# Optimization experiments

Hardware: AMD Instinct MI355X
Metric: run time of the kernel (lower is better)

## Reference

```python
import jax, jax.numpy as jnp
import numpy as np

N = 100000   # nodes
E = 1000000  # edges (avg degree 10)
F_IN, H1, H2, C = 128, 64, 64, 16


def setup_inputs() -> dict:
    key = jax.random.key(0)
    ks = jax.random.split(key, 10)
    x = jax.random.normal(ks[0], (N, F_IN), dtype=jnp.float32)
    edge_src = jax.random.randint(ks[1], (E,), 0, N, dtype=jnp.int32)
    edge_dst = jax.random.randint(ks[2], (E,), 0, N, dtype=jnp.int32)
    # normalized-adjacency-like positive edge weights (~1/deg scale)
    edge_val = jax.random.uniform(ks[3], (E,), dtype=jnp.float32) * 0.1
    def glorot(k, fan_in, fan_out):
        s = np.float32(1.0 / np.sqrt(fan_in))
        return jax.random.normal(k, (fan_in, fan_out), dtype=jnp.float32) * s
    W1 = glorot(ks[4], F_IN, H1)
    W2 = glorot(ks[5], H1, H2)
    W3 = glorot(ks[6], H2, C)
    b1 = jnp.zeros((H1,), jnp.float32)
    b2 = jnp.zeros((H2,), jnp.float32)
    b3 = jnp.zeros((C,), jnp.float32)
    return {"x": x, "edge_val": edge_val, "W1": W1, "b1": b1,
            "W2": W2, "b2": b2, "W3": W3, "b3": b3,
            "edge_src": edge_src, "edge_dst": edge_dst}


def gcn_layer(h, W, b, edge_src, edge_dst, edge_val):
    # support = h @ W ; out = spmm(adj, support) + b
    support = h @ W                                  # [N, d_out]
    msg = support[edge_src] * edge_val[:, None]      # [E, d_out] gather + scale
    agg = jax.ops.segment_sum(msg, edge_dst, num_segments=N)  # scatter-add
    return agg + b


def reference(x, edge_val, W1, b1, W2, b2, W3, b3, edge_src, edge_dst):
    # eval mode: F.dropout(training=False) is identity
    h = jax.nn.relu(gcn_layer(x, W1, b1, edge_src, edge_dst, edge_val))
    h = jax.nn.relu(gcn_layer(h, W2, b2, edge_src, edge_dst, edge_val))
    return gcn_layer(h, W3, b3, edge_src, edge_dst, edge_val)  # [N, C] logits
```

## Files before the change

kernel.cpp:

```cpp
#include <hip/hip_runtime.h>
#include <stdint.h>

#define N_NODES 100000
#define N_EDGES 1000000
#define NBUCK 98
#define CAP 12288

typedef __attribute__((ext_vector_type(8))) __bf16 bf16x8;
typedef __attribute__((ext_vector_type(4))) float f32x4;

static __device__ __forceinline__ float bf2f(unsigned short u) {
    return __uint_as_float(((unsigned int)u) << 16);
}
static __device__ __forceinline__ unsigned short f2bf(float f) {
    unsigned int u = __float_as_uint(f);
    unsigned int r = (u + 0x7FFFu + ((u >> 16) & 1u)) >> 16;
    return (unsigned short)r;
}
static __device__ __forceinline__ float4 ld4_half(const unsigned short* p) {
    ushort4 u = *(const ushort4*)p;
    return make_float4(bf2f(u.x), bf2f(u.y), bf2f(u.z), bf2f(u.w));
}
static __device__ __forceinline__ void st4_half(unsigned short* p, float4 f) {
    ushort4 u;
    u.x = f2bf(f.x); u.y = f2bf(f.y); u.z = f2bf(f.z); u.w = f2bf(f.w);
    *(ushort4*)p = u;
}
static __device__ __forceinline__ void st8_half(unsigned short* p, const float* f) {
    int4 u;
    u.x = (int)(((unsigned)f2bf(f[0])) | (((unsigned)f2bf(f[1])) << 16));
    u.y = (int)(((unsigned)f2bf(f[2])) | (((unsigned)f2bf(f[3])) << 16));
    u.z = (int)(((unsigned)f2bf(f[4])) | (((unsigned)f2bf(f[5])) << 16));
    u.w = (int)(((unsigned)f2bf(f[6])) | (((unsigned)f2bf(f[7])) << 16));
    *(int4*)p = u;
}

static __device__ __forceinline__ float ldf(const void* p, size_t i, int bf) {
    return bf ? bf2f(((const unsigned short*)p)[i]) : ((const float*)p)[i];
}
static __device__ __forceinline__ float4 ldf4(const void* p, size_t i, int bf) {
    if (bf) return ld4_half((const unsigned short*)p + i);
    return *(const float4*)((const float*)p + i);
}

__global__ __launch_bounds__(256) void detect_kernel(const unsigned short* __restrict__ xs,
                                                     int* __restrict__ flag,
                                                     int* __restrict__ bcursor) {
    __shared__ int sz;
    if (threadIdx.x == 0) sz = 0;
    __syncthreads();
    int z = 0;
    for (int i = threadIdx.x; i < 1024; i += 256) {
        float av = fabsf(bf2f(xs[2 * i]));
        if (!(av <= 1048576.0f) || (av != 0.0f && av < 9.5367431640625e-07f)) z++;
    }
    atomicAdd(&sz, z);
    if (threadIdx.x < NBUCK) bcursor[threadIdx.x] = threadIdx.x * CAP;
    __syncthreads();
    if (threadIdx.x == 0) *flag = (sz > 256) ? 0 : 1;
}

__global__ __launch_bounds__(256) void part_kernel(const int* __restrict__ src,
                                                   const int* __restrict__ dst,
                                                   const void* __restrict__ val,
                                                   int* __restrict__ bcursor,
                                                   int2* __restrict__ part,
                                                   const int* __restrict__ flagp) {
    __shared__ int cnt[NBUCK];
    __shared__ int base[NBUCK];
    const int bf = *flagp;
    const int tid = threadIdx.x;
    const int e0 = blockIdx.x * 2048;
    for (int i = tid; i < NBUCK; i += 256) cnt[i] = 0;
    __syncthreads();
    int rank[8], bkt[8], pk[8], vb[8];
#pragma unroll
    for (int i = 0; i < 8; ++i) {
        int e = e0 + i * 256 + tid;
        bkt[i] = -1;
        if (e < N_EDGES) {
            int d = dst[e];
            int b = d >> 10;
            bkt[i] = b;
            pk[i] = src[e] | ((d & 1023) << 17);
            vb[i] = __float_as_int(ldf(val, e, bf));
            rank[i] = atomicAdd(&cnt[b], 1);
        }
    }
    __syncthreads();
    for (int i = tid; i < NBUCK; i += 256) {
        int c = cnt[i];
        base[i] = c ? atomicAdd(&bcursor[i], c) : 0;
    }
    __syncthreads();
#pragma unroll
    for (int i = 0; i < 8; ++i) {
        if (bkt[i] >= 0) part[(size_t)base[bkt[i]] + rank[i]] = make_int2(pk[i], vb[i]);
    }
}

__global__ __launch_bounds__(512) void place_kernel(const int* __restrict__ bcursor,
                                                    const int2* __restrict__ part,
                                                    int* __restrict__ row_start,
                                                    int2* __restrict__ csr_rec) {
    __shared__ int cnt[1024];
    __shared__ int sums[512];
    __shared__ int sh_s, sh_cnt, sh_total;
    const int tid = threadIdx.x;
    const int b = blockIdx.x;
    const int row0 = b << 10;
    const int nrows = min(1024, N_NODES - row0);

    if (tid < 128) sums[tid] = (tid < NBUCK) ? (bcursor[tid] - tid * CAP) : 0;
    __syncthreads();
    for (int off = 1; off < 128; off <<= 1) {
        int t = 0;
        if (tid < 128 && tid >= off) t = sums[tid - off];
        __syncthreads();
        if (tid < 128 && tid >= off) sums[tid] += t;
        __syncthreads();
    }
    if (tid == 0) {
        sh_s = (b > 0) ? sums[b - 1] : 0;
        sh_cnt = bcursor[b] - b * CAP;
        sh_total = sums[NBUCK - 1];
    }
    __syncthreads();
    const int s = sh_s;
    const int cb = sh_cnt;
    const int ps = b * CAP;
    const int total = sh_total;

    for (int i = tid; i < 1024; i += 512) cnt[i] = 0;
    __syncthreads();
    for (int j = tid; j < cb; j += 512) {
        unsigned p = (unsigned)part[ps + j].x;
        atomicAdd(&cnt[p >> 17], 1);
    }
    __syncthreads();
    int a0 = cnt[2 * tid], a1 = cnt[2 * tid + 1];
    int ts = a0 + a1;
    sums[tid] = ts;
    __syncthreads();
    for (int off = 1; off < 512; off <<= 1) {
        int t = 0;
        if (tid >= off) t = sums[tid - off];
        __syncthreads();
        if (tid >= off) sums[tid] += t;
        __syncthreads();
    }
    int excl = sums[tid] - ts;
    cnt[2 * tid] = s + excl;
    cnt[2 * tid + 1] = s + excl + a0;
    if (2 * tid < nrows)     row_start[row0 + 2 * tid] = s + excl;
    if (2 * tid + 1 < nrows) row_start[row0 + 2 * tid + 1] = s + excl + a0;
    if (b == NBUCK - 1 && tid == 0) row_start[N_NODES] = total;
    __syncthreads();
    for (int j = tid; j < cb; j += 512) {
        int2 r = part[ps + j];
        unsigned p = (unsigned)r.x;
        int pos = atomicAdd(&cnt[p >> 17], 1);
        csr_rec[pos] = make_int2((int)(p & 0x1FFFFu), r.y);
    }
}

static __device__ __forceinline__ void duo_gather64(const unsigned short* __restrict__ supc,
                                                    const int2* __restrict__ csr_rec,
                                                    int s, int b1, int e,
                                                    float a0[8], float a1[8]) {
    if (s >= e) return;
    int2 r[8];
#pragma unroll
    for (int t = 0; t < 8; ++t) r[t] = csr_rec[min(s + t, e - 1)];
    for (int j = s; j < e; j += 8) {
        int4 sp[8];
#pragma unroll
        for (int t = 0; t < 8; ++t) sp[t] = *(const int4*)(supc + (size_t)r[t].x * 64);
        float wv[8];
#pragma unroll
        for (int t = 0; t < 8; ++t) wv[t] = (j + t < e) ? __int_as_float(r[t].y) : 0.0f;
        int jn = j + 8;
        if (jn < e) {
#pragma unroll
            for (int t = 0; t < 8; ++t) r[t] = csr_rec[min(jn + t, e - 1)];
        }
#pragma unroll
        for (int t = 0; t < 8; ++t) {
            float w0 = (j + t < b1) ? wv[t] : 0.0f;
            float w1 = wv[t] - w0;
            int q[4] = {sp[t].x, sp[t].y, sp[t].z, sp[t].w};
#pragma unroll
            for (int c = 0; c < 4; ++c) {
                float flo = __uint_as_float(((unsigned)q[c]) << 16);
                float fhi = __uint_as_float(((unsigned)q[c]) & 0xffff0000u);
                a0[2 * c]     += w0 * flo; a0[2 * c + 1] += w0 * fhi;
                a1[2 * c]     += w1 * flo; a1[2 * c + 1] += w1 * fhi;
            }
        }
    }
}

static __device__ __forceinline__ void quad_gather16(const unsigned short* __restrict__ supc,
                                                     const int2* __restrict__ csr_rec,
                                                     int s, int b1, int b2, int b3, int e,
                                                     float a[4][8]) {
    if (s >= e) return;
    int2 r[8];
#pragma unroll
    for (int t = 0; t < 8; ++t) r[t] = csr_rec[min(s + t, e - 1)];
    for (int j = s; j < e; j += 8) {
        int4 sp[8];
#pragma unroll
        for (int t = 0; t < 8; ++t) sp[t] = *(const int4*)(supc + (size_t)r[t].x * 16);
        float wv[8];
#pragma unroll
        for (int t = 0; t < 8; ++t) wv[t] = (j + t < e) ? __int_as_float(r[t].y) : 0.0f;
        int jn = j + 8;
        if (jn < e) {
#pragma unroll
            for (int t = 0; t < 8; ++t) r[t] = csr_rec[min(jn + t, e - 1)];
        }
#pragma unroll
        for (int t = 0; t < 8; ++t) {
            int idx = j + t;
            float c0 = (idx < b1) ? wv[t] : 0.0f;
            float c1 = (idx < b2) ? wv[t] : 0.0f;
            float c2 = (idx < b3) ? wv[t] : 0.0f;
            float w0 = c0, w1 = c1 - c0, w2 = c2 - c1, w3 = wv[t] - c2;
            int q[4] = {sp[t].x, sp[t].y, sp[t].z, sp[t].w};
#pragma unroll
            for (int c = 0; c < 4; ++c) {
                float flo = __uint_as_float(((unsigned)q[c]) << 16);
                float fhi = __uint_as_float(((unsigned)q[c]) & 0xffff0000u);
                a[0][2 * c] += w0 * flo; a[0][2 * c + 1] += w0 * fhi;
                a[1][2 * c] += w1 * flo; a[1][2 * c + 1] += w1 * fhi;
                a[2][2 * c] += w2 * flo; a[2][2 * c + 1] += w2 * fhi;
                a[3][2 * c] += w3 * flo; a[3][2 * c + 1] += w3 * fhi;
            }
        }
    }
}

template <int K, int M, bool DYNIN>
__global__ __launch_bounds__(256) void mgemm_kernel(const void* __restrict__ hv_,
                                                    const void* __restrict__ W,
                                                    unsigned short* __restrict__ out,
                                                    const int* __restrict__ flagp) {
    constexpr int KP = K + 8;
    constexpr int NC = M / 16;
    constexpr int NK = K / 32;

    __shared__ unsigned short wt[M][KP];

    const int bf = *flagp;
    const int tid = threadIdx.x;

    for (int i = tid; i < K * M; i += 256) {
        int k = i / M, m = i % M;
        wt[m][k] = f2bf(ldf(W, i, bf));
    }
    __syncthreads();

    const int lane = tid & 63;
    const int qd = lane >> 4;
    const int ln = lane & 15;
    const int wrow = (tid >> 6) * 16;
    const int tile = blockIdx.x;

    const int row = tile * 64 + wrow + ln;
    const bool ok = row < N_NODES;

    f32x4 acc[NC];
#pragma unroll
    for (int c = 0; c < NC; ++c) acc[c] = (f32x4){0.f, 0.f, 0.f, 0.f};

#pragma unroll
    for (int ks = 0; ks < NK; ++ks) {
        bf16x8 a;
        if (ok) {
            const size_t base = (size_t)row * K + ks * 32 + qd * 8;
            if (DYNIN && !bf) {
                const float* xp = (const float*)hv_ + base;
                float4 f0 = *(const float4*)xp;
                float4 f1 = *(const float4*)(xp + 4);
                ushort4 uu[2];
                uu[0].x = f2bf(f0.x); uu[0].y = f2bf(f0.y); uu[0].z = f2bf(f0.z); uu[0].w = f2bf(f0.w);
                uu[1].x = f2bf(f1.x); uu[1].y = f2bf(f1.y); uu[1].z = f2bf(f1.z); uu[1].w = f2bf(f1.w);
                a = *(const bf16x8*)uu;
            } else {
                a = *(const bf16x8*)((const unsigned short*)hv_ + base);
            }
        } else {
            a = (bf16x8)(__bf16)0.0f;
        }
#pragma unroll
        for (int c = 0; c < NC; ++c) {
            bf16x8 b = *(const bf16x8*)&wt[c * 16 + ln][ks * 32 + qd * 8];
            acc[c] = __builtin_amdgcn_mfma_f32_16x16x32_bf16(a, b, acc[c], 0, 0, 0);
        }
    }

#pragma unroll
    for (int c = 0; c < NC; ++c) {
#pragma unroll
        for (int r = 0; r < 4; ++r) {
            int orow = tile * 64 + wrow + qd * 4 + r;
            if (orow < N_NODES) out[(size_t)orow * M + c * 16 + ln] = f2bf(acc[c][r]);
        }
    }
}

template <int MOUT>
__global__ __launch_bounds__(256) void fused_kernel(const unsigned short* __restrict__ support,
                                                    const int* __restrict__ row_start,
                                                    const int2* __restrict__ csr_rec,
                                                    const void* __restrict__ bias,
                                                    const void* __restrict__ W,
                                                    unsigned short* __restrict__ out,
                                                    const int* __restrict__ flagp) {
    constexpr int K = 64, KP = 72;
    constexpr int NC = MOUT / 16;
    constexpr int NK = 2;

    __shared__ unsigned short agg[64][KP];
    __shared__ unsigned short wt[MOUT][KP];

    const int bf = *flagp;
    const int tid = threadIdx.x;

    for (int i = tid; i < K * MOUT; i += 256) {
        int k = i / MOUT, m = i % MOUT;
        wt[m][k] = f2bf(ldf(W, i, bf));
    }
    __syncthreads();

    const int lane = tid & 63;
    const int qd = lane >> 4;
    const int ln = lane & 15;
    const int wrow = (tid >> 6) * 16;

    const int grp = tid >> 3;
    const int cc = tid & 7;
    float bias8[8];
#pragma unroll
    for (int c = 0; c < 8; ++c) bias8[c] = ldf(bias, cc * 8 + c, bf);
    const unsigned short* supc = support + cc * 8;

    const int tile = blockIdx.x;
    const int r0 = tile * 64 + grp * 2;
    int s  = row_start[min(r0 + 0, N_NODES)];
    int b1 = row_start[min(r0 + 1, N_NODES)];
    int e  = row_start[min(r0 + 2, N_NODES)];

    float a0[8], a1[8];
#pragma unroll
    for (int c = 0; c < 8; ++c) { a0[c] = bias8[c]; a1[c] = bias8[c]; }
    duo_gather64(supc, csr_rec, s, b1, e, a0, a1);
#pragma unroll
    for (int c = 0; c < 8; ++c) {
        a0[c] = fmaxf(a0[c], 0.f);
        a1[c] = fmaxf(a1[c], 0.f);
    }
    st8_half(&agg[grp * 2 + 0][cc * 8], a0);
    st8_half(&agg[grp * 2 + 1][cc * 8], a1);
    __syncthreads();

    f32x4 macc[NC];
#pragma unroll
    for (int c = 0; c < NC; ++c) macc[c] = (f32x4){0.f, 0.f, 0.f, 0.f};
#pragma unroll
    for (int ks = 0; ks < NK; ++ks) {
        bf16x8 a = *(const bf16x8*)&agg[wrow + ln][ks * 32 + qd * 8];
#pragma unroll
        for (int c = 0; c < NC; ++c) {
            bf16x8 b = *(const bf16x8*)&wt[c * 16 + ln][ks * 32 + qd * 8];
            macc[c] = __builtin_amdgcn_mfma_f32_16x16x32_bf16(a, b, macc[c], 0, 0, 0);
        }
    }

#pragma unroll
    for (int c = 0; c < NC; ++c) {
#pragma unroll
        for (int r = 0; r < 4; ++r) {
            int orow = tile * 64 + wrow + qd * 4 + r;
            if (orow < N_NODES) out[(size_t)orow * MOUT + c * 16 + ln] = f2bf(macc[c][r]);
        }
    }
}

template <bool DYNOUT>
__global__ __launch_bounds__(256) void spmm16_kernel(const unsigned short* __restrict__ support,
                                                     const int* __restrict__ row_start,
                                                     const int2* __restrict__ csr_rec,
                                                     const void* __restrict__ bias,
                                                     void* __restrict__ out_,
                                                     const int* __restrict__ flagp) {
    constexpr int M = 16;
    int bf = *flagp;
    int tid = threadIdx.x;
    int grp = tid >> 1;
    int cc = tid & 1;
    int r0 = blockIdx.x * 512 + grp * 4;
    if (r0 >= N_NODES) return;
    int s  = row_start[min(r0 + 0, N_NODES)];
    int b1 = row_start[min(r0 + 1, N_NODES)];
    int b2 = row_start[min(r0 + 2, N_NODES)];
    int b3 = row_start[min(r0 + 3, N_NODES)];
    int e  = row_start[min(r0 + 4, N_NODES)];
    float a[4][8];
#pragma unroll
    for (int k = 0; k < 4; ++k)
#pragma unroll
        for (int c = 0; c < 8; ++c) a[k][c] = ldf(bias, cc * 8 + c, bf);
    quad_gather16(support + cc * 8, csr_rec, s, b1, b2, b3, e, a);
#pragma unroll
    for (int k = 0; k < 4; ++k) {
        int row = r0 + k;
        if (row < N_NODES) {
            if (DYNOUT && !bf) {
                float* op = (float*)out_ + (size_t)row * M + cc * 8;
                *(float4*)op = make_float4(a[k][0], a[k][1], a[k][2], a[k][3]);
                *(float4*)(op + 4) = make_float4(a[k][4], a[k][5], a[k][6], a[k][7]);
            } else {
                st8_half((unsigned short*)out_ + (size_t)row * M + cc * 8, a[k]);
            }
        }
    }
}

extern "C" void kernel_launch(void* const* d_in, const int* in_sizes, int n_in,
                              void* d_out, int out_size, void* d_ws, size_t ws_size,
                              hipStream_t stream) {
    (void)in_sizes; (void)n_in; (void)out_size; (void)ws_size;
    const void* x  = d_in[0];
    const void* ev = d_in[1];
    const void* W1 = d_in[2];
    const void* b1 = d_in[3];
    const void* W2 = d_in[4];
    const void* b2 = d_in[5];
    const void* W3 = d_in[6];
    const void* b3 = d_in[7];
    const int* esrc = (const int*)d_in[8];
    const int* edst = (const int*)d_in[9];

    char* ws = (char*)d_ws;
    size_t off = 0;
    auto alloc = [&](size_t bytes) -> void* {
        void* p = ws + off;
        off = (off + bytes + 255) & ~(size_t)255;
        return p;
    };
    unsigned short* A = (unsigned short*)alloc((size_t)N_NODES * 64 * 2);
    unsigned short* B = (unsigned short*)alloc((size_t)N_NODES * 64 * 2);
    int* row_start  = (int*)alloc((size_t)(N_NODES + 1) * 4);
    int* bcursor    = (int*)alloc(512);
    int2* csr_rec   = (int2*)alloc((size_t)N_EDGES * 8);
    int* flagp      = (int*)alloc(256);
    int2* part      = (int2*)A;

    detect_kernel<<<1, 256, 0, stream>>>((const unsigned short*)x, flagp, bcursor);

    part_kernel<<<(N_EDGES + 2047) / 2048, 256, 0, stream>>>(esrc, edst, ev, bcursor, part, flagp);
    place_kernel<<<NBUCK, 512, 0, stream>>>(bcursor, part, row_start, csr_rec);

    const int NT = (N_NODES + 63) / 64;

    mgemm_kernel<128, 64, true><<<NT, 256, 0, stream>>>(x, W1, A, flagp);
    fused_kernel<64><<<NT, 256, 0, stream>>>(A, row_start, csr_rec, b1, W2, B, flagp);
    fused_kernel<16><<<NT, 256, 0, stream>>>(B, row_start, csr_rec, b2, W3, A, flagp);
    spmm16_kernel<true><<<(N_NODES + 511) / 512, 256, 0, stream>>>(A, row_start, csr_rec, b3, d_out, flagp);
}
```

Before: 245.7 us.

## Gather one row per thread pair instead of masked multi-row accumulation

Replaces the duo/quad gather helpers with a single-row gather, templated on row stride and unrolled by 4 instead of 8. Each thread pair now accumulates only its own row, so the masked multi-row accumulators and their wasted FMAs go away. spmm16 moves from 512 to 128 rows per block, which quadruples the grid so the 16-wide last layer can fill more CUs. It also adds a launch_bounds occupancy hint of 8 and drops a redundant barrier after the weight fill in fused_kernel; the trade-off is less memory-level parallelism per thread and more, smaller blocks.

```diff
diff --git a/kernel.cpp b/kernel.cpp
--- a/kernel.cpp
+++ b/kernel.cpp
@@ -20,11 +20,6 @@
 static __device__ __forceinline__ float4 ld4_half(const unsigned short* p) {
     ushort4 u = *(const ushort4*)p;
     return make_float4(bf2f(u.x), bf2f(u.y), bf2f(u.z), bf2f(u.w));
-}
-static __device__ __forceinline__ void st4_half(unsigned short* p, float4 f) {
-    ushort4 u;
-    u.x = f2bf(f.x); u.y = f2bf(f.y); u.z = f2bf(f.z); u.w = f2bf(f.w);
-    *(ushort4*)p = u;
 }
 static __device__ __forceinline__ void st8_half(unsigned short* p, const float* f) {
     int4 u;
@@ -37,10 +32,6 @@
 
 static __device__ __forceinline__ float ldf(const void* p, size_t i, int bf) {
     return bf ? bf2f(((const unsigned short*)p)[i]) : ((const float*)p)[i];
-}
-static __device__ __forceinline__ float4 ldf4(const void* p, size_t i, int bf) {
-    if (bf) return ld4_half((const unsigned short*)p + i);
-    return *(const float4*)((const float*)p + i);
 }
 
 __global__ __launch_bounds__(256) void detect_kernel(const unsigned short* __restrict__ xs,
@@ -164,78 +155,36 @@
     }
 }
 
-static __device__ __forceinline__ void duo_gather64(const unsigned short* __restrict__ supc,
-                                                    const int2* __restrict__ csr_rec,
-                                                    int s, int b1, int e,
-                                                    float a0[8], float a1[8]) {
+template <int RS>
+static __device__ __forceinline__ void row_gather(const unsigned short* __restrict__ supc,
+                                                  const int2* __restrict__ csr_rec,
+                                                  int s, int e, float a[8]) {
     if (s >= e) return;
-    int2 r[8];
-#pragma unroll
-    for (int t = 0; t < 8; ++t) r[t] = csr_rec[min(s + t, e - 1)];
-    for (int j = s; j < e; j += 8) {
-        int4 sp[8];
-#pragma unroll
-        for (int t = 0; t < 8; ++t) sp[t] = *(const int4*)(supc + (size_t)r[t].x * 64);
-        float wv[8];
-#pragma unroll
-        for (int t = 0; t < 8; ++t) wv[t] = (j + t < e) ? __int_as_float(r[t].y) : 0.0f;
-        int jn = j + 8;
+    int2 r[4];
+#pragma unroll
+    for (int t = 0; t < 4; ++t) r[t] = csr_rec[min(s + t, e - 1)];
+    for (int j = s; j < e; j += 4) {
+        int4 sp[4];
+#pragma unroll
+        for (int t = 0; t < 4; ++t) sp[t] = *(const int4*)(supc + (size_t)r[t].x * RS);
+        float wv[4];
+#pragma unroll
+        for (int t = 0; t < 4; ++t) wv[t] = (j + t < e) ? __int_as_float(r[t].y) : 0.0f;
+        int jn = j + 4;
         if (jn < e) {
 #pragma unroll
-            for (int t = 0; t < 8; ++t) r[t] = csr_rec[min(jn + t, e - 1)];
-        }
-#pragma unroll
-        for (int t = 0; t < 8; ++t) {
-            float w0 = (j + t < b1) ? wv[t] : 0.0f;
-            float w1 = wv[t] - w0;
+            for (int t = 0; t < 4; ++t) r[t] = csr_rec[min(jn + t, e - 1)];
+        }
+#pragma unroll
+        for (int t = 0; t < 4; ++t) {
+            float w = wv[t];
             int q[4] = {sp[t].x, sp[t].y, sp[t].z, sp[t].w};
 #pragma unroll
             for (int c = 0; c < 4; ++c) {
                 float flo = __uint_as_float(((unsigned)q[c]) << 16);
                 float fhi = __uint_as_float(((unsigned)q[c]) & 0xffff0000u);
-                a0[2 * c]     += w0 * flo; a0[2 * c + 1] += w0 * fhi;
-                a1[2 * c]     += w1 * flo; a1[2 * c + 1] += w1 * fhi;
-            }
-        }
-    }
-}
-
-static __device__ __forceinline__ void quad_gather16(const unsigned short* __restrict__ supc,
-                                                     const int2* __restrict__ csr_rec,
-                                                     int s, int b1, int b2, int b3, int e,
-                                                     float a[4][8]) {
-    if (s >= e) return;
-    int2 r[8];
-#pragma unroll
-    for (int t = 0; t < 8; ++t) r[t] = csr_rec[min(s + t, e - 1)];
-    for (int j = s; j < e; j += 8) {
-        int4 sp[8];
-#pragma unroll
-        for (int t = 0; t < 8; ++t) sp[t] = *(const int4*)(supc + (size_t)r[t].x * 16);
-        float wv[8];
-#pragma unroll
-        for (int t = 0; t < 8; ++t) wv[t] = (j + t < e) ? __int_as_float(r[t].y) : 0.0f;
-        int jn = j + 8;
-        if (jn < e) {
-#pragma unroll
-            for (int t = 0; t < 8; ++t) r[t] = csr_rec[min(jn + t, e - 1)];
-        }
-#pragma unroll
-        for (int t = 0; t < 8; ++t) {
-            int idx = j + t;
-            float c0 = (idx < b1) ? wv[t] : 0.0f;
-            float c1 = (idx < b2) ? wv[t] : 0.0f;
-            float c2 = (idx < b3) ? wv[t] : 0.0f;
-            float w0 = c0, w1 = c1 - c0, w2 = c2 - c1, w3 = wv[t] - c2;
-            int q[4] = {sp[t].x, sp[t].y, sp[t].z, sp[t].w};
-#pragma unroll
-            for (int c = 0; c < 4; ++c) {
-                float flo = __uint_as_float(((unsigned)q[c]) << 16);
-                float fhi = __uint_as_float(((unsigned)q[c]) & 0xffff0000u);
-                a[0][2 * c] += w0 * flo; a[0][2 * c + 1] += w0 * fhi;
-                a[1][2 * c] += w1 * flo; a[1][2 * c + 1] += w1 * fhi;
-                a[2][2 * c] += w2 * flo; a[2][2 * c + 1] += w2 * fhi;
-                a[3][2 * c] += w3 * flo; a[3][2 * c + 1] += w3 * fhi;
+                a[2 * c]     += w * flo;
+                a[2 * c + 1] += w * fhi;
             }
         }
     }
@@ -311,13 +260,13 @@
 }
 
 template <int MOUT>
-__global__ __launch_bounds__(256) void fused_kernel(const unsigned short* __restrict__ support,
-                                                    const int* __restrict__ row_start,
-                                                    const int2* __restrict__ csr_rec,
-                                                    const void* __restrict__ bias,
-                                                    const void* __restrict__ W,
-                                                    unsigned short* __restrict__ out,
-                                                    const int* __restrict__ flagp) {
+__global__ __launch_bounds__(256, 8) void fused_kernel(const unsigned short* __restrict__ support,
+                                                       const int* __restrict__ row_start,
+                                                       const int2* __restrict__ csr_rec,
+                                                       const void* __restrict__ bias,
+                                                       const void* __restrict__ W,
+                                                       unsigned short* __restrict__ out,
+                                                       const int* __restrict__ flagp) {
     constexpr int K = 64, KP = 72;
     constexpr int NC = MOUT / 16;
     constexpr int NK = 2;
@@ -332,7 +281,6 @@
         int k = i / MOUT, m = i % MOUT;
         wt[m][k] = f2bf(ldf(W, i, bf));
     }
-    __syncthreads();
 
     const int lane = tid & 63;
     const int qd = lane >> 4;
@@ -347,22 +295,19 @@
     const unsigned short* supc = support + cc * 8;
 
     const int tile = blockIdx.x;
-    const int r0 = tile * 64 + grp * 2;
-    int s  = row_start[min(r0 + 0, N_NODES)];
-    int b1 = row_start[min(r0 + 1, N_NODES)];
-    int e  = row_start[min(r0 + 2, N_NODES)];
-
-    float a0[8], a1[8];
-#pragma unroll
-    for (int c = 0; c < 8; ++c) { a0[c] = bias8[c]; a1[c] = bias8[c]; }
-    duo_gather64(supc, csr_rec, s, b1, e, a0, a1);
-#pragma unroll
-    for (int c = 0; c < 8; ++c) {
-        a0[c] = fmaxf(a0[c], 0.f);
-        a1[c] = fmaxf(a1[c], 0.f);
-    }
-    st8_half(&agg[grp * 2 + 0][cc * 8], a0);
-    st8_half(&agg[grp * 2 + 1][cc * 8], a1);
+#pragma unroll
+    for (int p = 0; p < 2; ++p) {
+        const int row = tile * 64 + p * 32 + grp;
+        int s = row_start[min(row, N_NODES)];
+        int e = row_start[min(row + 1, N_NODES)];
+        float a[8];
+#pragma unroll
+        for (int c = 0; c < 8; ++c) a[c] = bias8[c];
+        row_gather<64>(supc, csr_rec, s, e, a);
+#pragma unroll
+        for (int c = 0; c < 8; ++c) a[c] = fmaxf(a[c], 0.f);
+        st8_half(&agg[p * 32 + grp][cc * 8], a);
+    }
     __syncthreads();
 
     f32x4 macc[NC];
@@ -389,42 +334,31 @@
 }
 
 template <bool DYNOUT>
-__global__ __launch_bounds__(256) void spmm16_kernel(const unsigned short* __restrict__ support,
-                                                     const int* __restrict__ row_start,
-                                                     const int2* __restrict__ csr_rec,
-                                                     const void* __restrict__ bias,
-                                                     void* __restrict__ out_,
-                                                     const int* __restrict__ flagp) {
+__global__ __launch_bounds__(256, 8) void spmm16_kernel(const unsigned short* __restrict__ support,
+                                                        const int* __restrict__ row_start,
+                                                        const int2* __restrict__ csr_rec,
+                                                        const void* __restrict__ bias,
+                                                        void* __restrict__ out_,
+                                                        const int* __restrict__ flagp) {
     constexpr int M = 16;
     int bf = *flagp;
     int tid = threadIdx.x;
     int grp = tid >> 1;
     int cc = tid & 1;
-    int r0 = blockIdx.x * 512 + grp * 4;
-    if (r0 >= N_NODES) return;
-    int s  = row_start[min(r0 + 0, N_NODES)];
-    int b1 = row_start[min(r0 + 1, N_NODES)];
-    int b2 = row_start[min(r0 + 2, N_NODES)];
-    int b3 = row_start[min(r0 + 3, N_NODES)];
-    int e  = row_start[min(r0 + 4, N_NODES)];
-    float a[4][8];
-#pragma unroll
-    for (int k = 0; k < 4; ++k)
-#pragma unroll
-        for (int c = 0; c < 8; ++c) a[k][c] = ldf(bias, cc * 8 + c, bf);
-    quad_gather16(support + cc * 8, csr_rec, s, b1, b2, b3, e, a);
-#pragma unroll
-    for (int k = 0; k < 4; ++k) {
-        int row = r0 + k;
-        if (row < N_NODES) {
-            if (DYNOUT && !bf) {
-                float* op = (float*)out_ + (size_t)row * M + cc * 8;
-                *(float4*)op = make_float4(a[k][0], a[k][1], a[k][2], a[k][3]);
-                *(float4*)(op + 4) = make_float4(a[k][4], a[k][5], a[k][6], a[k][7]);
-            } else {
-                st8_half((unsigned short*)out_ + (size_t)row * M + cc * 8, a[k]);
-            }
-        }
+    int row = blockIdx.x * 128 + grp;
+    if (row >= N_NODES) return;
+    int s = row_start[row];
+    int e = row_start[row + 1];
+    float a[8];
+#pragma unroll
+    for (int c = 0; c < 8; ++c) a[c] = ldf(bias, cc * 8 + c, bf);
+    row_gather<16>(support + cc * 8, csr_rec, s, e, a);
+    if (DYNOUT && !bf) {
+        float* op = (float*)out_ + (size_t)row * M + cc * 8;
+        *(float4*)op = make_float4(a[0], a[1], a[2], a[3]);
+        *(float4*)(op + 4) = make_float4(a[4], a[5], a[6], a[7]);
+    } else {
+        st8_half((unsigned short*)out_ + (size_t)row * M + cc * 8, a);
     }
 }
 
@@ -468,5 +402,5 @@
     mgemm_kernel<128, 64, true><<<NT, 256, 0, stream>>>(x, W1, A, flagp);
     fused_kernel<64><<<NT, 256, 0, stream>>>(A, row_start, csr_rec, b1, W2, B, flagp);
     fused_kernel<16><<<NT, 256, 0, stream>>>(B, row_start, csr_rec, b2, W3, A, flagp);
-    spmm16_kernel<true><<<(N_NODES + 511) / 512, 256, 0, stream>>>(A, row_start, csr_rec, b3, d_out, flagp);
-}
+    spmm16_kernel<true><<<(N_NODES + 127) / 128, 256, 0, stream>>>(A, row_start, csr_rec, b3, d_out, flagp);
+}
```

Result: faster. 229.2 us (-6.7%).
